# Kernel optimization log

Measured on AMD Instinct MI355X. Metric: run time of the kernel, lower is better.

## Reference

```python
import jax, jax.numpy as jnp
import numpy as np

B, EEG_D, FMRI_D, BD, H, NC = 131072, 128, 64, 128, 4, 2
HD = BD // H  # head dim = 32
EPS = 1e-5

def layernorm(x, g, b):
    m = jnp.mean(x, axis=-1, keepdims=True)
    v = jnp.var(x, axis=-1, keepdims=True)
    return (x - m) * jax.lax.rsqrt(v + EPS) * g + b

def setup_inputs() -> dict:
    key = jax.random.key(0)
    ks = jax.random.split(key, 24)
    r = lambda i, shape, s=0.05: jax.random.normal(ks[i], shape, dtype=jnp.float32) * s
    return {
        'eeg_feats': jax.random.normal(ks[0], (B, EEG_D), dtype=jnp.float32),
        'fmri_feats': jax.random.normal(ks[1], (B, FMRI_D), dtype=jnp.float32),
        # projections (weights stored [in, out])
        'We': r(2, (EEG_D, BD)), 'be': jnp.zeros((BD,)),
        'ge': jnp.ones((BD,)), 'bge': jnp.zeros((BD,)),
        'Wf': r(3, (FMRI_D, BD)), 'bf': jnp.zeros((BD,)),
        'gf': jnp.ones((BD,)), 'bgf': jnp.zeros((BD,)),
        # multihead attention
        'Wq': r(4, (BD, BD)), 'bq': jnp.zeros((BD,)),
        'Wk': r(5, (BD, BD)), 'bk': jnp.zeros((BD,)),
        'Wv': r(6, (BD, BD)), 'bv': jnp.zeros((BD,)),
        'Wo': r(7, (BD, BD)), 'bo': jnp.zeros((BD,)),
        # learned fusion
        'fusion_logits': jnp.zeros((2,)),
        'temperature': jnp.ones(()),
        # classifier
        'Wc1': r(8, (BD, BD // 2)), 'bc1': jnp.zeros((BD // 2,)),
        'gc': jnp.ones((BD // 2,)), 'bgc': jnp.zeros((BD // 2,)),
        'Wc2': r(9, (BD // 2, NC)), 'bc2': jnp.zeros((NC,)),
    }

def reference(eeg_feats, fmri_feats, We, be, ge, bge, Wf, bf, gf, bgf,
              Wq, bq, Wk, bk, Wv, bv, Wo, bo, fusion_logits, temperature,
              Wc1, bc1, gc, bgc, Wc2, bc2):
    # modality projections: Linear + LN + GELU (dropout off at eval)
    eeg_p = jax.nn.gelu(layernorm(eeg_feats @ We + be, ge, bge), approximate=False)
    fmri_p = jax.nn.gelu(layernorm(fmri_feats @ Wf + bf, gf, bgf), approximate=False)

    # cross-attention: query = eeg_p (1 token), kv = [eeg_p, fmri_p] (2 tokens)
    seq = jnp.stack([eeg_p, fmri_p], axis=1)                 # [B, 2, BD]
    q = (eeg_p @ Wq + bq).reshape(B, H, HD)                  # [B, H, HD]
    k = (seq @ Wk + bk).reshape(B, 2, H, HD)
    v = (seq @ Wv + bv).reshape(B, 2, H, HD)
    scores = jnp.einsum('bhd,bkhd->bhk', q, k) / jnp.sqrt(jnp.float32(HD))
    attn = jax.nn.softmax(scores, axis=-1)                   # [B, H, 2]
    ctx = jnp.einsum('bhk,bkhd->bhd', attn, v).reshape(B, BD)
    eeg_enh = ctx @ Wo + bo                                  # [B, BD]

    # learned temperature-scaled fusion over [eeg_enhanced, fmri_proj]
    w = jax.nn.softmax(fusion_logits / temperature, axis=0)
    fused = w[0] * eeg_enh + w[1] * fmri_p                   # [B, BD]

    # classifier: Linear + LN + ReLU + Linear
    h = jax.nn.relu(layernorm(fused @ Wc1 + bc1, gc, bgc))
    logits = h @ Wc2 + bc2                                   # [B, NC]
    return logits
```

## Files before the change

### kernel.cpp

```cpp
#include <hip/hip_runtime.h>
#include <math.h>

#define EPS 1e-5f
#define SCALE 0.17677669529663687f

#define OFF_We  0
#define OFF_Wf  16384
#define OFF_Wq  24576
#define OFF_Wk  40960
#define OFF_Wv  57344
#define OFF_Wo  73728
#define OFF_Wc1 90112
#define PACK_TOTAL 98304

#define CHUNK 8192

typedef __bf16 bf16x8 __attribute__((ext_vector_type(8)));
typedef float f32x4 __attribute__((ext_vector_type(4)));
typedef unsigned short ushort_t;
typedef unsigned short ushortx4 __attribute__((ext_vector_type(4)));

__device__ __forceinline__ ushort_t f2bf(float x) {
    unsigned u = __builtin_bit_cast(unsigned, x);
    u = (u + 0x7fffu + ((u >> 16) & 1u)) >> 16;
    return (ushort_t)u;
}
__device__ __forceinline__ float bf2f(ushort_t v) {
    unsigned u = ((unsigned)v) << 16;
    return __builtin_bit_cast(float, u);
}

#define DPPADD(x, ctrl) \
    ((x) + __builtin_bit_cast(float, __builtin_amdgcn_update_dpp( \
        __builtin_bit_cast(int, (x)), __builtin_bit_cast(int, (x)), (ctrl), 0xF, 0xF, false)))

__device__ __forceinline__ float rowsum16(float x) {
    x = DPPADD(x, 0x121);
    x = DPPADD(x, 0x122);
    x = DPPADD(x, 0x124);
    x = DPPADD(x, 0x128);
    return x;
}

__device__ __forceinline__ float gelu_fast(float x) {
    float x2 = x * x;
    float u = x * fmaf(0.07135481283f, x2, 1.5957691216f);
    float e = __expf(-u);
    return x * __builtin_amdgcn_rcpf(1.0f + e);
}

__global__ __launch_bounds__(256) void pack_all(
    const float* __restrict__ We, const float* __restrict__ Wf,
    const float* __restrict__ Wq, const float* __restrict__ Wk,
    const float* __restrict__ Wv, const float* __restrict__ Wo,
    const float* __restrict__ Wc1, ushort_t* __restrict__ ws)
{
    int o = blockIdx.x * 256 + threadIdx.x;
    if (o >= PACK_TOTAL) return;
    const float* W; int K, N, base;
    if (o < OFF_Wf)        { W = We;  K = 128; N = 128; base = OFF_We; }
    else if (o < OFF_Wq)   { W = Wf;  K = 64;  N = 128; base = OFF_Wf; }
    else if (o < OFF_Wk)   { W = Wq;  K = 128; N = 128; base = OFF_Wq; }
    else if (o < OFF_Wv)   { W = Wk;  K = 128; N = 128; base = OFF_Wk; }
    else if (o < OFF_Wo)   { W = Wv;  K = 128; N = 128; base = OFF_Wv; }
    else if (o < OFF_Wc1)  { W = Wo;  K = 128; N = 128; base = OFF_Wo; }
    else                   { W = Wc1; K = 128; N = 64;  base = OFF_Wc1; }
    int e = o - base;
    int j = e & 7, l = (e >> 3) & 63, rest = e >> 9;
    int KS = K >> 5;
    int s = rest % KS, t = rest / KS;
    int k = s * 32 + ((l >> 4) << 3) + j;
    int n = (t << 4) + (l & 15);
    ws[o] = f2bf(W[k * N + n]);
}

template<int KS>
__device__ __forceinline__ void load_af(bf16x8 af[KS], const ushort_t* A, int lane)
{
    const int quad = lane >> 4, l16 = lane & 15;
    #pragma unroll
    for (int ks = 0; ks < KS; ++ks)
        af[ks] = *(const bf16x8*)(A + l16 * 136 + ks * 32 + quad * 8);
}

template<int KS, int NT4>
__device__ __forceinline__ void mma_c(const bf16x8 af[KS], const ushort_t* sW,
                                      f32x4* acc, int lane)
{
    #pragma unroll
    for (int t = 0; t < NT4; ++t)
        #pragma unroll
        for (int ks = 0; ks < KS; ++ks) {
            bf16x8 bb = *(const bf16x8*)(sW + ((t * KS + ks) * 64 + lane) * 8);
            acc[t] = __builtin_amdgcn_mfma_f32_16x16x32_bf16(af[ks], bb, acc[t], 0, 0, 0);
        }
}

__global__ __launch_bounds__(256, 3) void fusion_stage(
    const float* __restrict__ eeg, const float* __restrict__ fmri,
    const float* __restrict__ be, const float* __restrict__ ge, const float* __restrict__ bge,
    const float* __restrict__ bfb, const float* __restrict__ gf, const float* __restrict__ bgf,
    const float* __restrict__ bq, const float* __restrict__ bk, const float* __restrict__ bv,
    const float* __restrict__ bo,
    const float* __restrict__ fusion_logits, const float* __restrict__ temperature,
    const float* __restrict__ bc1, const float* __restrict__ gc, const float* __restrict__ bgc,
    const float* __restrict__ Wc2, const float* __restrict__ bc2,
    const ushort_t* __restrict__ ws, float* __restrict__ out)
{
    __shared__ __align__(16) ushort_t sW[CHUNK];
    __shared__ __align__(16) ushort_t B1[4][16 * 136];
    __shared__ __align__(16) ushort_t B2[4][16 * 136];

    const int tid = threadIdx.x;
    const int wave = tid >> 6, lane = tid & 63;
    const int quad = lane >> 4, l16 = lane & 15;
    const int rowbase = blockIdx.x * 64 + wave * 16;
    ushort_t* b1 = B1[wave];
    ushort_t* b2 = B2[wave];

    auto stageW = [&](int offU) {
        __syncthreads();
        const uint4* g = (const uint4*)(ws + offU);
        uint4* d = (uint4*)sW;
        #pragma unroll
        for (int i = 0; i < 4; ++i) d[tid + i * 256] = g[tid + i * 256];
        __syncthreads();
    };

    {
        const float4* src = (const float4*)(eeg + (size_t)rowbase * 128);
        #pragma unroll
        for (int i = 0; i < 8; ++i) {
            int idx = i * 64 + lane;
            float4 v = src[idx];
            int r = idx >> 5, k4 = (idx & 31) * 4;
            *(ushortx4*)&b1[r * 136 + k4] =
                (ushortx4){f2bf(v.x), f2bf(v.y), f2bf(v.z), f2bf(v.w)};
        }
        const float4* srcf = (const float4*)(fmri + (size_t)rowbase * 64);
        #pragma unroll
        for (int i = 0; i < 4; ++i) {
            int idx = i * 64 + lane;
            float4 v = srcf[idx];
            int r = idx >> 4, k4 = (idx & 15) * 4;
            *(ushortx4*)&b2[r * 136 + k4] =
                (ushortx4){f2bf(v.x), f2bf(v.y), f2bf(v.z), f2bf(v.w)};
        }
    }

    float meanS[4], rstdS[4];

    {
        bf16x8 afR[4]; load_af<4>(afR, b1, lane);
        f32x4 acc[8];
        #pragma unroll
        for (int nt = 0; nt < 8; ++nt) {
            float b = be[nt * 16 + l16];
            acc[nt] = (f32x4){b, b, b, b};
        }
        stageW(OFF_We);          mma_c<4, 4>(afR, sW, acc + 0, lane);
        stageW(OFF_We + CHUNK);  mma_c<4, 4>(afR, sW, acc + 4, lane);
        #pragma unroll
        for (int r = 0; r < 4; ++r) {
            float s = 0.f, ss = 0.f;
            #pragma unroll
            for (int nt = 0; nt < 8; ++nt) { float x = acc[nt][r]; s += x; ss = fmaf(x, x, ss); }
            s = rowsum16(s); ss = rowsum16(ss);
            float m = s * (1.f / 128.f);
            meanS[r] = m;
            rstdS[r] = rsqrtf(ss * (1.f / 128.f) - m * m + EPS);
        }
        #pragma unroll
        for (int nt = 0; nt < 8; ++nt) {
            float g = ge[nt * 16 + l16], bb = bge[nt * 16 + l16];
            #pragma unroll
            for (int r = 0; r < 4; ++r) {
                float x = (acc[nt][r] - meanS[r]) * rstdS[r] * g + bb;
                b1[(quad * 4 + r) * 136 + nt * 16 + l16] = f2bf(gelu_fast(x));
            }
        }
    }

    {
        bf16x8 afR[2]; load_af<2>(afR, b2, lane);
        f32x4 acc[8];
        #pragma unroll
        for (int nt = 0; nt < 8; ++nt) {
            float b = bfb[nt * 16 + l16];
            acc[nt] = (f32x4){b, b, b, b};
        }
        stageW(OFF_Wf);  mma_c<2, 8>(afR, sW, acc, lane);
        #pragma unroll
        for (int r = 0; r < 4; ++r) {
            float s = 0.f, ss = 0.f;
            #pragma unroll
            for (int nt = 0; nt < 8; ++nt) { float x = acc[nt][r]; s += x; ss = fmaf(x, x, ss); }
            s = rowsum16(s); ss = rowsum16(ss);
            float m = s * (1.f / 128.f);
            meanS[r] = m;
            rstdS[r] = rsqrtf(ss * (1.f / 128.f) - m * m + EPS);
        }
        #pragma unroll
        for (int nt = 0; nt < 8; ++nt) {
            float g = gf[nt * 16 + l16], bb = bgf[nt * 16 + l16];
            #pragma unroll
            for (int r = 0; r < 4; ++r) {
                float x = (acc[nt][r] - meanS[r]) * rstdS[r] * g + bb;
                b2[(quad * 4 + r) * 136 + nt * 16 + l16] = f2bf(gelu_fast(x));
            }
        }
    }

    bf16x8 afE[4]; load_af<4>(afE, b1, lane);
    bf16x8 afF[4]; load_af<4>(afF, b2, lane);

    f32x4 q[8];
    {
        #pragma unroll
        for (int nt = 0; nt < 8; ++nt) {
            float b = bq[nt * 16 + l16];
            q[nt] = (f32x4){b, b, b, b};
        }
        stageW(OFF_Wq);          mma_c<4, 4>(afE, sW, q + 0, lane);
        stageW(OFF_Wq + CHUNK);  mma_c<4, 4>(afE, sW, q + 4, lane);
    }

    float a0v[4][4];
    {
        float pd[4][4];
        #pragma unroll
        for (int h = 0; h < 4; ++h)
            #pragma unroll
            for (int r = 0; r < 4; ++r) pd[h][r] = 0.f;
        #pragma unroll
        for (int c = 0; c < 2; ++c) {
            stageW(OFF_Wk + c * CHUNK);
            #pragma unroll
            for (int tl = 0; tl < 4; ++tl) {
                int nt = c * 4 + tl;
                f32x4 e = {0.f, 0.f, 0.f, 0.f}, f = {0.f, 0.f, 0.f, 0.f};
                #pragma unroll
                for (int ks = 0; ks < 4; ++ks) {
                    bf16x8 bb = *(const bf16x8*)(sW + ((tl * 4 + ks) * 64 + lane) * 8);
                    e = __builtin_amdgcn_mfma_f32_16x16x32_bf16(afE[ks], bb, e, 0, 0, 0);
                    f = __builtin_amdgcn_mfma_f32_16x16x32_bf16(afF[ks], bb, f, 0, 0, 0);
                }
                int h = nt >> 1;
                #pragma unroll
                for (int r = 0; r < 4; ++r)
                    pd[h][r] = fmaf(q[nt][r], e[r] - f[r], pd[h][r]);
            }
        }
        #pragma unroll
        for (int h = 0; h < 4; ++h)
            #pragma unroll
            for (int r = 0; r < 4; ++r) {
                float d = rowsum16(pd[h][r]) * SCALE;
                a0v[h][r] = __builtin_amdgcn_rcpf(1.0f + __expf(-d));
            }
    }

    #pragma unroll
    for (int c = 0; c < 2; ++c) {
        stageW(OFF_Wv + c * CHUNK);
        #pragma unroll
        for (int tl = 0; tl < 4; ++tl) {
            int nt = c * 4 + tl;
            float b = bv[nt * 16 + l16];
            f32x4 e = {b, b, b, b}, f = {b, b, b, b};
            #pragma unroll
            for (int ks = 0; ks < 4; ++ks) {
                bf16x8 bb = *(const bf16x8*)(sW + ((tl * 4 + ks) * 64 + lane) * 8);
                e = __builtin_amdgcn_mfma_f32_16x16x32_bf16(afE[ks], bb, e, 0, 0, 0);
                f = __builtin_amdgcn_mfma_f32_16x16x32_bf16(afF[ks], bb, f, 0, 0, 0);
            }
            int h = nt >> 1;
            #pragma unroll
            for (int r = 0; r < 4; ++r) {
                float a0 = a0v[h][r];
                float c0 = a0 * e[r] + (1.0f - a0) * f[r];
                b1[(quad * 4 + r) * 136 + nt * 16 + l16] = f2bf(c0);
            }
        }
    }

    {
        bf16x8 afC[4]; load_af<4>(afC, b1, lane);
        f32x4 acc[8];
        #pragma unroll
        for (int nt = 0; nt < 8; ++nt) {
            float b = bo[nt * 16 + l16];
            acc[nt] = (f32x4){b, b, b, b};
        }
        stageW(OFF_Wo);          mma_c<4, 4>(afC, sW, acc + 0, lane);
        stageW(OFF_Wo + CHUNK);  mma_c<4, 4>(afC, sW, acc + 4, lane);
        float t = temperature[0];
        float dl = (fusion_logits[0] - fusion_logits[1]) / t;
        float w0 = __builtin_amdgcn_rcpf(1.0f + __expf(-dl));
        float w1 = 1.0f - w0;
        #pragma unroll
        for (int nt = 0; nt < 8; ++nt)
            #pragma unroll
            for (int r = 0; r < 4; ++r) {
                int off = (quad * 4 + r) * 136 + nt * 16 + l16;
                float fp = bf2f(b2[off]);
                b1[off] = f2bf(w0 * acc[nt][r] + w1 * fp);
            }
    }

    {
        bf16x8 afU[4]; load_af<4>(afU, b1, lane);
        f32x4 accH[4];
        #pragma unroll
        for (int nt = 0; nt < 4; ++nt) {
            float b = bc1[nt * 16 + l16];
            accH[nt] = (f32x4){b, b, b, b};
        }
        stageW(OFF_Wc1);  mma_c<4, 4>(afU, sW, accH, lane);
        #pragma unroll
        for (int r = 0; r < 4; ++r) {
            float s = 0.f, ss = 0.f;
            #pragma unroll
            for (int nt = 0; nt < 4; ++nt) { float x = accH[nt][r]; s += x; ss = fmaf(x, x, ss); }
            s = rowsum16(s); ss = rowsum16(ss);
            float m = s * (1.f / 64.f);
            meanS[r] = m;
            rstdS[r] = rsqrtf(ss * (1.f / 64.f) - m * m + EPS);
        }
        float hv[4][4];
        #pragma unroll
        for (int nt = 0; nt < 4; ++nt) {
            float g = gc[nt * 16 + l16], bb = bgc[nt * 16 + l16];
            #pragma unroll
            for (int r = 0; r < 4; ++r) {
                float x = (accH[nt][r] - meanS[r]) * rstdS[r] * g + bb;
                hv[nt][r] = fmaxf(x, 0.0f);
            }
        }
        float w2v[4][2];
        #pragma unroll
        for (int nt = 0; nt < 4; ++nt) {
            float2 w = *(const float2*)&Wc2[(nt * 16 + l16) * 2];
            w2v[nt][0] = w.x; w2v[nt][1] = w.y;
        }
        float o0c = bc2[0], o1c = bc2[1];
        #pragma unroll
        for (int r = 0; r < 4; ++r) {
            float p0 = 0.f, p1 = 0.f;
            #pragma unroll
            for (int nt = 0; nt < 4; ++nt) {
                p0 = fmaf(hv[nt][r], w2v[nt][0], p0);
                p1 = fmaf(hv[nt][r], w2v[nt][1], p1);
            }
            p0 = rowsum16(p0); p1 = rowsum16(p1);
            if (l16 == 0) {
                int row = rowbase + quad * 4 + r;
                float2 o; o.x = p0 + o0c; o.y = p1 + o1c;
                *(float2*)&out[row * 2] = o;
            }
        }
    }
}

extern "C" void kernel_launch(void* const* d_in, const int* in_sizes, int n_in,
                              void* d_out, int out_size, void* d_ws, size_t ws_size,
                              hipStream_t stream) {
    const float* eeg  = (const float*)d_in[0];
    const float* fmri = (const float*)d_in[1];
    const float* We   = (const float*)d_in[2];
    const float* be   = (const float*)d_in[3];
    const float* ge   = (const float*)d_in[4];
    const float* bge  = (const float*)d_in[5];
    const float* Wf   = (const float*)d_in[6];
    const float* bf   = (const float*)d_in[7];
    const float* gf   = (const float*)d_in[8];
    const float* bgf  = (const float*)d_in[9];
    const float* Wq   = (const float*)d_in[10];
    const float* bq   = (const float*)d_in[11];
    const float* Wk   = (const float*)d_in[12];
    const float* bk   = (const float*)d_in[13];
    const float* Wv   = (const float*)d_in[14];
    const float* bv   = (const float*)d_in[15];
    const float* Wo   = (const float*)d_in[16];
    const float* bo   = (const float*)d_in[17];
    const float* fl   = (const float*)d_in[18];
    const float* temp = (const float*)d_in[19];
    const float* Wc1  = (const float*)d_in[20];
    const float* bc1  = (const float*)d_in[21];
    const float* gc   = (const float*)d_in[22];
    const float* bgc  = (const float*)d_in[23];
    const float* Wc2  = (const float*)d_in[24];
    const float* bc2  = (const float*)d_in[25];
    float* out = (float*)d_out;
    ushort_t* ws = (ushort_t*)d_ws;

    hipLaunchKernelGGL(pack_all, dim3((PACK_TOTAL + 255) / 256), dim3(256), 0, stream,
                       We, Wf, Wq, Wk, Wv, Wo, Wc1, ws);

    int B = in_sizes[0] / 128;
    int grid = B / 64;
    hipLaunchKernelGGL(fusion_stage, dim3(grid), dim3(256), 0, stream,
                       eeg, fmri, be, ge, bge, bf, gf, bgf,
                       bq, bk, bv, bo, fl, temp, bc1, gc, bgc, Wc2, bc2,
                       ws, out);
}
```

Baseline: 210.7 us.

## Use direct global-to-LDS weight staging, hardware bf16 convert, and register-held fMRI projection

After: 204.8 us. -2.8%, faster.

```diff
diff --git a/kernel.cpp b/kernel.cpp
--- a/kernel.cpp
+++ b/kernel.cpp
@@ -21,13 +21,17 @@
 typedef unsigned short ushortx4 __attribute__((ext_vector_type(4)));
 
 __device__ __forceinline__ ushort_t f2bf(float x) {
+    return __builtin_bit_cast(ushort_t, (__bf16)x);
+}
+__device__ __forceinline__ float bf2f(ushort_t v) {
+    unsigned u = ((unsigned)v) << 16;
+    return __builtin_bit_cast(float, u);
+}
+
+__device__ __forceinline__ ushort_t f2bf_sw(float x) {
     unsigned u = __builtin_bit_cast(unsigned, x);
     u = (u + 0x7fffu + ((u >> 16) & 1u)) >> 16;
     return (ushort_t)u;
-}
-__device__ __forceinline__ float bf2f(ushort_t v) {
-    unsigned u = ((unsigned)v) << 16;
-    return __builtin_bit_cast(float, u);
 }
 
 #define DPPADD(x, ctrl) \
@@ -44,8 +48,12 @@
 
 __device__ __forceinline__ float gelu_fast(float x) {
     float x2 = x * x;
-    float u = x * fmaf(0.07135481283f, x2, 1.5957691216f);
-    float e = __expf(-u);
+    float t = fmaf(-0.10294313843f, x2, -2.30220842f);
+#if __has_builtin(__builtin_amdgcn_exp2f)
+    float e = __builtin_amdgcn_exp2f(x * t);
+#else
+    float e = __expf(x * t * 0.6931471806f);
+#endif
     return x * __builtin_amdgcn_rcpf(1.0f + e);
 }
 
@@ -60,7 +68,7 @@
     const float* W; int K, N, base;
     if (o < OFF_Wf)        { W = We;  K = 128; N = 128; base = OFF_We; }
     else if (o < OFF_Wq)   { W = Wf;  K = 64;  N = 128; base = OFF_Wf; }
-    else if (o < OFF_Wk)   { W = Wq;  K = 128; N = 128; base = OFF_Wq; }
+    else if (o < OFF_Wk)   { W = Wq;  K = 128; N = 128; base = OFF_Wk == OFF_Wk ? OFF_Wq : OFF_Wq; }
     else if (o < OFF_Wv)   { W = Wk;  K = 128; N = 128; base = OFF_Wk; }
     else if (o < OFF_Wo)   { W = Wv;  K = 128; N = 128; base = OFF_Wv; }
     else if (o < OFF_Wc1)  { W = Wo;  K = 128; N = 128; base = OFF_Wo; }
@@ -71,7 +79,7 @@
     int s = rest % KS, t = rest / KS;
     int k = s * 32 + ((l >> 4) << 3) + j;
     int n = (t << 4) + (l & 15);
-    ws[o] = f2bf(W[k * N + n]);
+    ws[o] = f2bf_sw(W[k * N + n]);
 }
 
 template<int KS>
@@ -120,10 +128,13 @@
 
     auto stageW = [&](int offU) {
         __syncthreads();
-        const uint4* g = (const uint4*)(ws + offU);
-        uint4* d = (uint4*)sW;
-        #pragma unroll
-        for (int i = 0; i < 4; ++i) d[tid + i * 256] = g[tid + i * 256];
+        const char* g = (const char*)(ws + offU) + tid * 16;
+        char* l = (char*)sW + tid * 16;
+        #pragma unroll
+        for (int i = 0; i < 4; ++i)
+            __builtin_amdgcn_global_load_lds(
+                (const __attribute__((address_space(1))) void*)(g + i * 4096),
+                (__attribute__((address_space(3))) void*)(l + i * 4096), 16, 0, 0);
         __syncthreads();
     };
 
@@ -181,6 +192,7 @@
         }
     }
 
+    f32x4 fpv[8];
     {
         bf16x8 afR[2]; load_af<2>(afR, b2, lane);
         f32x4 acc[8];
@@ -206,7 +218,9 @@
             #pragma unroll
             for (int r = 0; r < 4; ++r) {
                 float x = (acc[nt][r] - meanS[r]) * rstdS[r] * g + bb;
-                b2[(quad * 4 + r) * 136 + nt * 16 + l16] = f2bf(gelu_fast(x));
+                float gv = gelu_fast(x);
+                fpv[nt][r] = gv;
+                b2[(quad * 4 + r) * 136 + nt * 16 + l16] = f2bf(gv);
             }
         }
     }
@@ -277,8 +291,7 @@
             int h = nt >> 1;
             #pragma unroll
             for (int r = 0; r < 4; ++r) {
-                float a0 = a0v[h][r];
-                float c0 = a0 * e[r] + (1.0f - a0) * f[r];
+                float c0 = fmaf(a0v[h][r], e[r] - f[r], f[r]);
                 b1[(quad * 4 + r) * 136 + nt * 16 + l16] = f2bf(c0);
             }
         }
@@ -303,8 +316,7 @@
             #pragma unroll
             for (int r = 0; r < 4; ++r) {
                 int off = (quad * 4 + r) * 136 + nt * 16 + l16;
-                float fp = bf2f(b2[off]);
-                b1[off] = f2bf(w0 * acc[nt][r] + w1 * fp);
+                b1[off] = f2bf(w0 * acc[nt][r] + w1 * fpv[nt][r]);
             }
     }
 
```
